# Kernel tuning notes

Hardware: AMD Instinct MI355X
Metric: run time of the kernel (lower is better)

## Reference

```python
import jax, jax.numpy as jnp
import numpy as np

MARGIN = 0.5
EPS = 1e-5
NOISE_RATE = 0.5


def setup_inputs() -> dict:
    key = jax.random.key(0)
    k1, k2, k3, k4, k5 = jax.random.split(key, 5)
    n, m, d, c = 1024, 65536, 512, 10000
    return {
        "inputs_col": jax.random.normal(k1, (n, d), dtype=jnp.float32),
        "inputs_row": jax.random.normal(k2, (m, d), dtype=jnp.float32),
        "center": jax.random.normal(k3, (c, d), dtype=jnp.float32),
        "targets_col": jax.random.randint(k4, (n,), 0, c, dtype=jnp.int64),
        "target_row": jax.random.randint(k5, (m,), 0, c, dtype=jnp.int64),
        "filled_mask": jnp.ones((c,), dtype=bool),
    }


def _prism_keep(features, targets, center, filled_mask, noise_rate):
    # no_grad in the original -> stop_gradient here
    f = jax.lax.stop_gradient(features)
    c = jax.lax.stop_gradient(center)
    # all_sim_exp[cls] / sum(all_sim_exp) is exactly softmax over class logits
    probs = jax.nn.softmax(f @ c.T, axis=-1)          # [n, num_classes]
    sel = jnp.take_along_axis(probs, targets[:, None], axis=1)[:, 0]  # [n]
    C = jnp.where(filled_mask[targets], sel, 1.0)      # not-in-memory -> 1
    n = C.shape[0]
    n_remove = int(noise_rate * n)                     # static
    to_remove = jnp.argsort(C)[:n_remove]
    # empty margin_window path: keep everything except to_remove
    keep = jnp.ones((n,), dtype=bool).at[to_remove].set(False)
    return keep


def reference(inputs_col, inputs_row, center, targets_col, target_row, filled_mask):
    n = inputs_col.shape[0]
    sim = inputs_col @ inputs_row.T                    # [n, m]
    pos_mask = targets_col[:, None] == target_row[None, :]
    neg_mask = (~pos_mask) & (sim > MARGIN)
    pos_mask = pos_mask & (sim < 1.0 - EPS)

    keep = _prism_keep(inputs_col, targets_col, center, filled_mask, NOISE_RATE)
    pos_mask = pos_mask & keep[:, None]
    neg_mask = neg_mask & keep[:, None]

    # sum over selected pairs without boolean-indexing (masked reductions)
    pos_loss = jnp.sum(jnp.where(pos_mask, 1.0 - sim, 0.0))
    neg_loss = jnp.sum(jnp.where(neg_mask, sim, 0.0))
    loss = (pos_loss + neg_loss) / n
    return loss, keep
```

## Files before the change

### kernel.cpp

```cpp
#include <hip/hip_runtime.h>


typedef int    v4i   __attribute__((ext_vector_type(4)));
typedef float  f32x4 __attribute__((ext_vector_type(4)));
typedef unsigned char u8;

#define N_COL  1024
#define M_ROW  65536
#define DDIM   512
#define NCLS   10000
#define NT     79
#define NREM   512

#define OFF_A8   0u
#define OFF_C8   524288u
#define OFF_PMS  39256064u
#define OFF_LT   39903232u
#define OFF_COMP 39907328u
#define OFF_TCC  39909376u
#define OFF_ACC  39911424u
#define OFF_CNT  39911432u

__device__ __forceinline__ void async16(const void* g, void* l) {
    __builtin_amdgcn_global_load_lds(
        (const __attribute__((address_space(1))) void*)g,
        (__attribute__((address_space(3))) void*)l, 16, 0, 0);
}

__device__ __forceinline__ unsigned pack4_fp8(float4 v) {
    int r = 0;
    r = __builtin_amdgcn_cvt_pk_fp8_f32(v.x, v.y, r, false);
    r = __builtin_amdgcn_cvt_pk_fp8_f32(v.z, v.w, r, true);
    return (unsigned)r;
}

__device__ __forceinline__ void gemm8_128(const u8* __restrict__ A,
                                          const u8* __restrict__ B,
                                          int m0, int n0,
                                          u8* As, u8* Bs, f32x4 (&acc)[4][4]) {
    const int tid = threadIdx.x, wid = tid >> 6, lane = tid & 63;
    const int wm = wid >> 1, wn = wid & 1;
    const int q = lane >> 4, lc = lane & 15;

    const u8* gA[4]; const u8* gB[4]; int voff[4];
#pragma unroll
    for (int s = 0; s < 4; ++s) {
        const int c  = wid * 256 + s * 64 + lane;
        const int r  = c >> 3;
        const int gs = (c & 7) ^ (r & 7);
        gA[s] = A + (size_t)(m0 + r) * DDIM + gs * 16;
        gB[s] = B + (size_t)(n0 + r) * DDIM + gs * 16;
        voff[s] = c * 16;
    }
#pragma unroll
    for (int i = 0; i < 4; ++i)
#pragma unroll
        for (int j = 0; j < 4; ++j) acc[i][j] = (f32x4){0.f, 0.f, 0.f, 0.f};

    for (int kt = 0; kt < 4; ++kt) {
        const int kb = kt * 128;
#pragma unroll
        for (int s = 0; s < 4; ++s) {
            async16(gA[s] + kb, As + voff[s]);
            async16(gB[s] + kb, Bs + voff[s]);
        }
        __syncthreads();
#pragma unroll
        for (int ks = 0; ks < 4; ++ks) {
            const int gg = ks * 2 + (q >> 1);
            const int bo = (q & 1) * 8;
            long long af[4], bv[4];
#pragma unroll
            for (int i = 0; i < 4; ++i) {
                const int rA = wm * 64 + i * 16 + lc;
                af[i] = *(const long long*)(As + (rA * 8 + (gg ^ (rA & 7))) * 16 + bo);
                const int rB = wn * 64 + i * 16 + lc;
                bv[i] = *(const long long*)(Bs + (rB * 8 + (gg ^ (rB & 7))) * 16 + bo);
            }
#pragma unroll
            for (int i = 0; i < 4; ++i)
#pragma unroll
                for (int j = 0; j < 4; ++j)
                    acc[i][j] = __builtin_amdgcn_mfma_f32_16x16x32_fp8_fp8(
                        af[i], bv[j], acc[i][j], 0, 0, 0);
        }
        __syncthreads();
    }
}

__global__ void k_prep(const float4* __restrict__ a4, const float4* __restrict__ c4,
                       const float* __restrict__ a32, const float* __restrict__ c32,
                       const int* __restrict__ tcol,
                       unsigned* __restrict__ A8w, uint2* __restrict__ C8w,
                       float* __restrict__ lt, double* __restrict__ accd,
                       unsigned* __restrict__ cnt) {
    const int b = blockIdx.x, tid = threadIdx.x;
    if (b == 0 && tid == 0) { *accd = 0.0; *cnt = 0u; }
    if (b < 256) {
        const int idx = b * 256 + tid;
        A8w[idx * 2]     = pack4_fp8(a4[idx * 2]);
        A8w[idx * 2 + 1] = pack4_fp8(a4[idx * 2 + 1]);
    } else if (b < 2784) {
        const int cidx = (b - 256) * 256 + tid;
        const int row  = cidx >> 6;
        uint2 o = make_uint2(0u, 0u);
        if (row < NCLS) {
            o.x = pack4_fp8(c4[cidx * 2]);
            o.y = pack4_fp8(c4[cidx * 2 + 1]);
        }
        C8w[cidx] = o;
    } else {
        const int w = (b - 2784) * 4 + (tid >> 6), lane = tid & 63;
        const int t = tcol[w];
        const float* ar = a32 + (size_t)w * DDIM;
        const float* cr = c32 + (size_t)t * DDIM;
        float s = 0.f;
#pragma unroll
        for (int k = 0; k < DDIM / 64; ++k) s += ar[lane + k * 64] * cr[lane + k * 64];
        for (int off = 32; off; off >>= 1) s += __shfl_down(s, off, 64);
        if (lane == 0) lt[w] = s;
    }
}

__global__ __launch_bounds__(256, 3) void k_mid(const u8* __restrict__ A8,
                                                const u8* __restrict__ C8,
                                                float2* __restrict__ pms) {
    const int b = blockIdx.x, tid = threadIdx.x;
    __shared__ __align__(16) u8 As[16384], Bs[16384];
    __shared__ float s_mm[128][2], s_ss[128][2];
    const int n_t = b >> 3, m0 = (b & 7) * 128, n0 = n_t * 128;
    f32x4 acc[4][4];
    gemm8_128(A8, C8, m0, n0, As, Bs, acc);

    const int wid = tid >> 6, lane = tid & 63;
    const int wm = wid >> 1, wn = wid & 1, q = lane >> 4, lc = lane & 15;
    const int cbase = n0 + wn * 64 + lc;
#pragma unroll
    for (int i = 0; i < 4; ++i) {
#pragma unroll
        for (int reg = 0; reg < 4; ++reg) {
            float mm = -INFINITY, ss = 0.f;
#pragma unroll
            for (int j = 0; j < 4; ++j)
                if (cbase + j * 16 < NCLS) mm = fmaxf(mm, acc[i][j][reg]);
#pragma unroll
            for (int j = 0; j < 4; ++j)
                if (cbase + j * 16 < NCLS) ss += __expf(acc[i][j][reg] - mm);
#pragma unroll
            for (int d2 = 1; d2 < 16; d2 <<= 1) {
                float mo = __shfl_xor(mm, d2, 16);
                float so = __shfl_xor(ss, d2, 16);
                float M = fmaxf(mm, mo), S = 0.f;
                if (ss > 0.f) S += ss * __expf(mm - M);
                if (so > 0.f) S += so * __expf(mo - M);
                mm = M; ss = S;
            }
            if (lc == 0) {
                const int row = i * 16 + q * 4 + reg;
                s_mm[wm * 64 + row][wn] = mm;
                s_ss[wm * 64 + row][wn] = ss;
            }
        }
    }
    __syncthreads();
    if (tid < 128) {
        float m1 = s_mm[tid][0], s1 = s_ss[tid][0];
        float m2 = s_mm[tid][1], s2 = s_ss[tid][1];
        float M = fmaxf(m1, m2), S = 0.f;
        if (s1 > 0.f) S += s1 * __expf(m1 - M);
        if (s2 > 0.f) S += s2 * __expf(m2 - M);
        pms[(size_t)n_t * N_COL + m0 + tid] = make_float2(M, S);
    }
}

__global__ __launch_bounds__(1024) void k_sel(const float2* __restrict__ pms,
                                              const float* __restrict__ lt,
                                              const int* __restrict__ tcol,
                                              int* __restrict__ comp,
                                              int* __restrict__ tcc,
                                              float* __restrict__ keep_out) {
    __shared__ float v[N_COL];
    const int i = threadIdx.x;
    float M = -INFINITY, S = 0.f;
    for (int t = 0; t < NT; ++t) {
        float2 p = pms[(size_t)t * N_COL + i];
        if (p.y > 0.f) {
            if (p.x > M) { S = S * __expf(M - p.x) + p.y; M = p.x; }
            else         { S += p.y * __expf(p.x - M); }
        }
    }
    const float x = lt[i] - (M + logf(S));
    v[i] = x;
    __syncthreads();
    int rank = 0;
    const float4* v4 = (const float4*)v;
#pragma unroll 8
    for (int j4 = 0; j4 < N_COL / 4; ++j4) {
        float4 w = v4[j4];
        const int j = j4 * 4;
        rank += (w.x < x) || (w.x == x && j     < i);
        rank += (w.y < x) || (w.y == x && j + 1 < i);
        rank += (w.z < x) || (w.z == x && j + 2 < i);
        rank += (w.w < x) || (w.w == x && j + 3 < i);
    }
    const bool keep = rank >= NREM;
    keep_out[i] = keep ? 1.0f : 0.0f;
    if (keep) { comp[rank - NREM] = i; tcc[rank - NREM] = tcol[i]; }
}

__global__ __launch_bounds__(512, 2) void k_loss(const u8* __restrict__ A8,
                                                 const float4* __restrict__ brow4,
                                                 const int* __restrict__ comp,
                                                 const int* __restrict__ tcc,
                                                 const int* __restrict__ trow,
                                                 double* __restrict__ accd,
                                                 unsigned* __restrict__ cnt,
                                                 float* __restrict__ out) {
    __shared__ __align__(16) u8 As[2][32768];
    __shared__ __align__(16) u8 Bs[2][8192];
    __shared__ int s_map[512], s_tc[512], s_tr[128];
    __shared__ float s_red[8];
    const int b = blockIdx.x, tid = threadIdx.x;
    const int n0 = b * 128;
    s_map[tid] = comp[tid];
    s_tc[tid]  = tcc[tid];
    if (tid < 128) s_tr[tid] = trow[n0 + tid];
    __syncthreads();

    const int wid = tid >> 6, lane = tid & 63;
    const int wm = wid >> 1, wn = wid & 1;
    const int q = lane >> 4, lc = lane & 15;

    const u8* gA[4]; int vA[4];
#pragma unroll
    for (int s = 0; s < 4; ++s) {
        const int cc = s * 512 + tid;
        const int r  = cc >> 2, gs = (cc & 3) ^ (r & 3);
        gA[s] = A8 + (size_t)s_map[r] * DDIM + gs * 16;
        vA[s] = cc * 16;
    }
    const int rB0 = tid >> 2, gB0 = tid & 3;
    const float4* gB = brow4 + (size_t)(n0 + rB0) * (DDIM / 4) + gB0 * 4;
    const int vB = (rB0 * 4 + (gB0 ^ (rB0 & 3))) * 16;

    f32x4 acc[8][4];
#pragma unroll
    for (int i = 0; i < 8; ++i)
#pragma unroll
        for (int j = 0; j < 4; ++j) acc[i][j] = (f32x4){0.f, 0.f, 0.f, 0.f};

    auto compute = [&](const u8* Asc, const u8* Bsc) {
#pragma unroll
        for (int ks = 0; ks < 2; ++ks) {
            const int gg = ks * 2 + (q >> 1);
            const int bo = (q & 1) * 8;
            long long af[8], bv[4];
#pragma unroll
            for (int i = 0; i < 8; ++i) {
                const int rA = wm * 128 + i * 16 + lc;
                af[i] = *(const long long*)(Asc + (rA * 4 + (gg ^ (rA & 3))) * 16 + bo);
            }
#pragma unroll
            for (int j = 0; j < 4; ++j) {
                const int rB = wn * 64 + j * 16 + lc;
                bv[j] = *(const long long*)(Bsc + (rB * 4 + (gg ^ (rB & 3))) * 16 + bo);
            }
#pragma unroll
            for (int i = 0; i < 8; ++i)
#pragma unroll
                for (int j = 0; j < 4; ++j)
                    acc[i][j] = __builtin_amdgcn_mfma_f32_16x16x32_fp8_fp8(
                        af[i], bv[j], acc[i][j], 0, 0, 0);
        }
    };

    {
#pragma unroll
        for (int s = 0; s < 4; ++s) async16(gA[s], As[0] + vA[s]);
        float4 f0 = gB[0], f1 = gB[1], f2 = gB[2], f3 = gB[3];
        uint4 pk;
        pk.x = pack4_fp8(f0); pk.y = pack4_fp8(f1);
        pk.z = pack4_fp8(f2); pk.w = pack4_fp8(f3);
        *(uint4*)(Bs[0] + vB) = pk;
        __syncthreads();
    }
    int cur = 0;
    for (int kt = 0; kt < 7; ++kt) {
        const int nxt = cur ^ 1;
        const int kb  = (kt + 1) * 64;
#pragma unroll
        for (int s = 0; s < 4; ++s) async16(gA[s] + kb, As[nxt] + vA[s]);
        const float4* gb = gB + (size_t)(kt + 1) * 16;
        float4 f0 = gb[0], f1 = gb[1], f2 = gb[2], f3 = gb[3];

        compute(As[cur], Bs[cur]);

        uint4 pk;
        pk.x = pack4_fp8(f0); pk.y = pack4_fp8(f1);
        pk.z = pack4_fp8(f2); pk.w = pack4_fp8(f3);
        *(uint4*)(Bs[nxt] + vB) = pk;
        __syncthreads();
        cur = nxt;
    }
    compute(As[cur], Bs[cur]);

    const float POSMAX = 1.0f - 1e-5f;
    float local = 0.f;
#pragma unroll
    for (int i = 0; i < 8; ++i) {
#pragma unroll
        for (int j = 0; j < 4; ++j) {
            const int tr = s_tr[wn * 64 + j * 16 + lc];
#pragma unroll
            for (int reg = 0; reg < 4; ++reg) {
                const int row = wm * 128 + i * 16 + q * 4 + reg;
                const float sim = acc[i][j][reg];
                if (s_tc[row] == tr) {
                    if (sim < POSMAX) local += 1.0f - sim;
                } else if (sim > 0.5f) {
                    local += sim;
                }
            }
        }
    }
    for (int off = 32; off; off >>= 1) local += __shfl_down(local, off, 64);
    if (lane == 0) s_red[wid] = local;
    __syncthreads();
    if (tid == 0) {
        float blk = 0.f;
#pragma unroll
        for (int w = 0; w < 8; ++w) blk += s_red[w];
        atomicAdd(accd, (double)blk);
        __threadfence();
        if (atomicAdd(cnt, 1u) == 511u) {
            double vfin = atomicAdd(accd, 0.0);
            out[0] = (float)(vfin / (double)N_COL);
        }
    }
}

extern "C" void kernel_launch(void* const* d_in, const int* in_sizes, int n_in,
                              void* d_out, int out_size, void* d_ws, size_t ws_size,
                              hipStream_t stream) {
    (void)in_sizes; (void)n_in; (void)out_size; (void)ws_size;
    const float* inputs_col  = (const float*)d_in[0];
    const float* inputs_row  = (const float*)d_in[1];
    const float* center      = (const float*)d_in[2];
    const int*   targets_col = (const int*)d_in[3];
    const int*   target_row  = (const int*)d_in[4];
    float* out = (float*)d_out;
    char*  ws  = (char*)d_ws;

    u8*       A8   = (u8*)(ws + OFF_A8);
    u8*       C8   = (u8*)(ws + OFF_C8);
    float2*   pms  = (float2*)(ws + OFF_PMS);
    float*    lt   = (float*) (ws + OFF_LT);
    int*      comp = (int*)   (ws + OFF_COMP);
    int*      tcc  = (int*)   (ws + OFF_TCC);
    double*   accd = (double*)(ws + OFF_ACC);
    unsigned* cnt  = (unsigned*)(ws + OFF_CNT);

    k_prep<<<3040, 256, 0, stream>>>((const float4*)inputs_col, (const float4*)center,
                                     inputs_col, center, targets_col,
                                     (unsigned*)A8, (uint2*)C8, lt, accd, cnt);
    k_mid<<<632, 256, 0, stream>>>(A8, C8, pms);
    k_sel<<<1, 1024, 0, stream>>>(pms, lt, targets_col, comp, tcc, out + 1);
    k_loss<<<512, 512, 0, stream>>>(A8, (const float4*)inputs_row,
                                    comp, tcc, target_row, accd, cnt, out);
}
```

Measured before the change: 332.4 us.

## Triple-buffer A tiles with prefetch distance two and change LDS swizzle

The fp8 GEMM main loop now keeps three shared-memory buffers for the A tiles and two register buffers for the B rows, so tiles are issued two k-steps ahead. Explicit vmcnt and lgkmcnt waits with raw s_barrier replace __syncthreads, and the loop is fully unrolled. The XOR swizzle of the 16-byte groups now uses (row>>1)&3 instead of row&3, to reduce LDS bank conflicts on the 8-byte fragment reads. The aim is to hide global-load latency behind MFMA work. The catch is that the extra 32KB A buffer raises LDS per block to about 114KB, which may allow only one block per CU instead of the two requested by launch_bounds.

```diff
diff --git a/kernel.cpp b/kernel.cpp
--- a/kernel.cpp
+++ b/kernel.cpp
@@ -216,7 +216,7 @@
                                                  double* __restrict__ accd,
                                                  unsigned* __restrict__ cnt,
                                                  float* __restrict__ out) {
-    __shared__ __align__(16) u8 As[2][32768];
+    __shared__ __align__(16) u8 As[3][32768];
     __shared__ __align__(16) u8 Bs[2][8192];
     __shared__ int s_map[512], s_tc[512], s_tr[128];
     __shared__ float s_red[8];
@@ -235,13 +235,14 @@
 #pragma unroll
     for (int s = 0; s < 4; ++s) {
         const int cc = s * 512 + tid;
-        const int r  = cc >> 2, gs = (cc & 3) ^ (r & 3);
-        gA[s] = A8 + (size_t)s_map[r] * DDIM + gs * 16;
+        const int r  = cc >> 2, gpos = cc & 3;
+        const int g  = gpos ^ ((r >> 1) & 3);
+        gA[s] = A8 + (size_t)s_map[r] * DDIM + g * 16;
         vA[s] = cc * 16;
     }
     const int rB0 = tid >> 2, gB0 = tid & 3;
     const float4* gB = brow4 + (size_t)(n0 + rB0) * (DDIM / 4) + gB0 * 4;
-    const int vB = (rB0 * 4 + (gB0 ^ (rB0 & 3))) * 16;
+    const int vB = (rB0 * 4 + (gB0 ^ ((rB0 >> 1) & 3))) * 16;
 
     f32x4 acc[8][4];
 #pragma unroll
@@ -258,12 +259,12 @@
 #pragma unroll
             for (int i = 0; i < 8; ++i) {
                 const int rA = wm * 128 + i * 16 + lc;
-                af[i] = *(const long long*)(Asc + (rA * 4 + (gg ^ (rA & 3))) * 16 + bo);
+                af[i] = *(const long long*)(Asc + (rA * 4 + (gg ^ ((rA >> 1) & 3))) * 16 + bo);
             }
 #pragma unroll
             for (int j = 0; j < 4; ++j) {
                 const int rB = wn * 64 + j * 16 + lc;
-                bv[j] = *(const long long*)(Bsc + (rB * 4 + (gg ^ (rB & 3))) * 16 + bo);
+                bv[j] = *(const long long*)(Bsc + (rB * 4 + (gg ^ ((rB >> 1) & 3))) * 16 + bo);
             }
 #pragma unroll
             for (int i = 0; i < 8; ++i)
@@ -274,35 +275,53 @@
         }
     };
 
+    float4 fb[2][4];
+
+#pragma unroll
+    for (int s = 0; s < 4; ++s) async16(gA[s], As[0] + vA[s]);
+#pragma unroll
+    for (int g = 0; g < 4; ++g) fb[0][g] = gB[g];
+    __builtin_amdgcn_sched_barrier(0);
+#pragma unroll
+    for (int s = 0; s < 4; ++s) async16(gA[s] + 64, As[1] + vA[s]);
+#pragma unroll
+    for (int g = 0; g < 4; ++g) fb[1][g] = gB[16 + g];
+    asm volatile("s_waitcnt vmcnt(8)" ::: "memory");
+    __builtin_amdgcn_sched_barrier(0);
     {
-#pragma unroll
-        for (int s = 0; s < 4; ++s) async16(gA[s], As[0] + vA[s]);
-        float4 f0 = gB[0], f1 = gB[1], f2 = gB[2], f3 = gB[3];
         uint4 pk;
-        pk.x = pack4_fp8(f0); pk.y = pack4_fp8(f1);
-        pk.z = pack4_fp8(f2); pk.w = pack4_fp8(f3);
+        pk.x = pack4_fp8(fb[0][0]); pk.y = pack4_fp8(fb[0][1]);
+        pk.z = pack4_fp8(fb[0][2]); pk.w = pack4_fp8(fb[0][3]);
         *(uint4*)(Bs[0] + vB) = pk;
-        __syncthreads();
-    }
-    int cur = 0;
-    for (int kt = 0; kt < 7; ++kt) {
-        const int nxt = cur ^ 1;
-        const int kb  = (kt + 1) * 64;
-#pragma unroll
-        for (int s = 0; s < 4; ++s) async16(gA[s] + kb, As[nxt] + vA[s]);
-        const float4* gb = gB + (size_t)(kt + 1) * 16;
-        float4 f0 = gb[0], f1 = gb[1], f2 = gb[2], f3 = gb[3];
-
-        compute(As[cur], Bs[cur]);
-
-        uint4 pk;
-        pk.x = pack4_fp8(f0); pk.y = pack4_fp8(f1);
-        pk.z = pack4_fp8(f2); pk.w = pack4_fp8(f3);
-        *(uint4*)(Bs[nxt] + vB) = pk;
-        __syncthreads();
-        cur = nxt;
-    }
-    compute(As[cur], Bs[cur]);
+    }
+    asm volatile("s_waitcnt lgkmcnt(0)" ::: "memory");
+    __builtin_amdgcn_s_barrier();
+
+#pragma unroll
+    for (int kt = 0; kt < 8; ++kt) {
+        if (kt < 6) {
+            const int kb = (kt + 2) * 64;
+#pragma unroll
+            for (int s = 0; s < 4; ++s) async16(gA[s] + kb, As[(kt + 2) % 3] + vA[s]);
+#pragma unroll
+            for (int g = 0; g < 4; ++g) fb[kt & 1][g] = gB[(kt + 2) * 16 + g];
+            asm volatile("s_waitcnt vmcnt(8)" ::: "memory");
+        } else if (kt == 6) {
+            asm volatile("s_waitcnt vmcnt(0)" ::: "memory");
+        }
+        __builtin_amdgcn_sched_barrier(0);
+        if (kt < 7) {
+            uint4 pk;
+            pk.x = pack4_fp8(fb[(kt + 1) & 1][0]); pk.y = pack4_fp8(fb[(kt + 1) & 1][1]);
+            pk.z = pack4_fp8(fb[(kt + 1) & 1][2]); pk.w = pack4_fp8(fb[(kt + 1) & 1][3]);
+            *(uint4*)(Bs[(kt + 1) & 1] + vB) = pk;
+        }
+        compute(As[kt % 3], Bs[kt & 1]);
+        if (kt < 7) {
+            asm volatile("s_waitcnt lgkmcnt(0)" ::: "memory");
+            __builtin_amdgcn_s_barrier();
+        }
+    }
 
     const float POSMAX = 1.0f - 1e-5f;
     float local = 0.f;
```

After: 337.3 us. No clear change (+1.5%).

## Raise loss-kernel occupancy, change LDS swizzle, add MFMA priority hints

Applied to the files above, without the earlier changes.

Raises launch bounds from 2 to 4 blocks per CU for the fused GEMM-loss kernel. Drops the shared-memory staging of the index and label arrays: labels are read straight from global memory into registers, and the reduction scratch reuses the A tile buffer. Changes the LDS XOR swizzle to key on row>>1 to cut bank conflicts for the 8-byte fragment reads. Also fully unrolls the k-loop and wraps the MFMA block in s_setprio. The tighter register budget (acc alone is 128 VGPRs) risks spills, and the 80KB of LDS per block may still cap how many blocks fit per CU.

```diff
diff --git a/kernel.cpp b/kernel.cpp
--- a/kernel.cpp
+++ b/kernel.cpp
@@ -208,7 +208,7 @@
     if (keep) { comp[rank - NREM] = i; tcc[rank - NREM] = tcol[i]; }
 }
 
-__global__ __launch_bounds__(512, 2) void k_loss(const u8* __restrict__ A8,
+__global__ __launch_bounds__(512, 4) void k_loss(const u8* __restrict__ A8,
                                                  const float4* __restrict__ brow4,
                                                  const int* __restrict__ comp,
                                                  const int* __restrict__ tcc,
@@ -218,14 +218,8 @@
                                                  float* __restrict__ out) {
     __shared__ __align__(16) u8 As[2][32768];
     __shared__ __align__(16) u8 Bs[2][8192];
-    __shared__ int s_map[512], s_tc[512], s_tr[128];
-    __shared__ float s_red[8];
     const int b = blockIdx.x, tid = threadIdx.x;
     const int n0 = b * 128;
-    s_map[tid] = comp[tid];
-    s_tc[tid]  = tcc[tid];
-    if (tid < 128) s_tr[tid] = trow[n0 + tid];
-    __syncthreads();
 
     const int wid = tid >> 6, lane = tid & 63;
     const int wm = wid >> 1, wn = wid & 1;
@@ -235,13 +229,14 @@
 #pragma unroll
     for (int s = 0; s < 4; ++s) {
         const int cc = s * 512 + tid;
-        const int r  = cc >> 2, gs = (cc & 3) ^ (r & 3);
-        gA[s] = A8 + (size_t)s_map[r] * DDIM + gs * 16;
+        const int r  = cc >> 2, gpos = cc & 3;
+        const int g  = gpos ^ ((r >> 1) & 3);
+        gA[s] = A8 + (size_t)comp[r] * DDIM + g * 16;
         vA[s] = cc * 16;
     }
     const int rB0 = tid >> 2, gB0 = tid & 3;
     const float4* gB = brow4 + (size_t)(n0 + rB0) * (DDIM / 4) + gB0 * 4;
-    const int vB = (rB0 * 4 + (gB0 ^ (rB0 & 3))) * 16;
+    const int vB = (rB0 * 4 + (gB0 ^ ((rB0 >> 1) & 3))) * 16;
 
     f32x4 acc[8][4];
 #pragma unroll
@@ -258,19 +253,21 @@
 #pragma unroll
             for (int i = 0; i < 8; ++i) {
                 const int rA = wm * 128 + i * 16 + lc;
-                af[i] = *(const long long*)(Asc + (rA * 4 + (gg ^ (rA & 3))) * 16 + bo);
+                af[i] = *(const long long*)(Asc + (rA * 4 + (gg ^ ((rA >> 1) & 3))) * 16 + bo);
             }
 #pragma unroll
             for (int j = 0; j < 4; ++j) {
                 const int rB = wn * 64 + j * 16 + lc;
-                bv[j] = *(const long long*)(Bsc + (rB * 4 + (gg ^ (rB & 3))) * 16 + bo);
-            }
+                bv[j] = *(const long long*)(Bsc + (rB * 4 + (gg ^ ((rB >> 1) & 3))) * 16 + bo);
+            }
+            __builtin_amdgcn_s_setprio(1);
 #pragma unroll
             for (int i = 0; i < 8; ++i)
 #pragma unroll
                 for (int j = 0; j < 4; ++j)
                     acc[i][j] = __builtin_amdgcn_mfma_f32_16x16x32_fp8_fp8(
                         af[i], bv[j], acc[i][j], 0, 0, 0);
+            __builtin_amdgcn_s_setprio(0);
         }
     };
 
@@ -284,38 +281,43 @@
         *(uint4*)(Bs[0] + vB) = pk;
         __syncthreads();
     }
-    int cur = 0;
+#pragma unroll
     for (int kt = 0; kt < 7; ++kt) {
-        const int nxt = cur ^ 1;
-        const int kb  = (kt + 1) * 64;
-#pragma unroll
-        for (int s = 0; s < 4; ++s) async16(gA[s] + kb, As[nxt] + vA[s]);
+        const int kb = (kt + 1) * 64;
+#pragma unroll
+        for (int s = 0; s < 4; ++s) async16(gA[s] + kb, As[(kt + 1) & 1] + vA[s]);
         const float4* gb = gB + (size_t)(kt + 1) * 16;
         float4 f0 = gb[0], f1 = gb[1], f2 = gb[2], f3 = gb[3];
 
-        compute(As[cur], Bs[cur]);
+        compute(As[kt & 1], Bs[kt & 1]);
 
         uint4 pk;
         pk.x = pack4_fp8(f0); pk.y = pack4_fp8(f1);
         pk.z = pack4_fp8(f2); pk.w = pack4_fp8(f3);
-        *(uint4*)(Bs[nxt] + vB) = pk;
+        *(uint4*)(Bs[(kt + 1) & 1] + vB) = pk;
         __syncthreads();
-        cur = nxt;
-    }
-    compute(As[cur], Bs[cur]);
+    }
+    compute(As[1], Bs[1]);
+    __syncthreads();
+
+    int trj[4];
+#pragma unroll
+    for (int j = 0; j < 4; ++j) trj[j] = trow[n0 + wn * 64 + j * 16 + lc];
 
     const float POSMAX = 1.0f - 1e-5f;
     float local = 0.f;
 #pragma unroll
     for (int i = 0; i < 8; ++i) {
+        int tcr[4];
+#pragma unroll
+        for (int reg = 0; reg < 4; ++reg)
+            tcr[reg] = tcc[wm * 128 + i * 16 + q * 4 + reg];
 #pragma unroll
         for (int j = 0; j < 4; ++j) {
-            const int tr = s_tr[wn * 64 + j * 16 + lc];
 #pragma unroll
             for (int reg = 0; reg < 4; ++reg) {
-                const int row = wm * 128 + i * 16 + q * 4 + reg;
                 const float sim = acc[i][j][reg];
-                if (s_tc[row] == tr) {
+                if (tcr[reg] == trj[j]) {
                     if (sim < POSMAX) local += 1.0f - sim;
                 } else if (sim > 0.5f) {
                     local += sim;
@@ -324,6 +326,7 @@
         }
     }
     for (int off = 32; off; off >>= 1) local += __shfl_down(local, off, 64);
+    float* s_red = (float*)As;
     if (lane == 0) s_red[wid] = local;
     __syncthreads();
     if (tid == 0) {
```

Result: slower. 619.5 us (+86.3%).

## Fuse keep-rank selection into loss kernel and change LDS swizzle pattern

Applied to the files above, without the earlier changes.

The single-block selection kernel is split up. A small 16-block kernel now computes per-row log-softmax values, and every loss block recomputes the O(n^2) rank selection redundantly in shared memory to build its compacted row map, with block 0 writing the keep mask. This removes the serialized one-block launch and its global round trip, at the cost of duplicated rank work in all 512 loss blocks and more shared memory per block. The LDS XOR swizzle is also changed from (r&3) to ((r>>1)&3) to alter bank-conflict behavior for the 8-byte fragment reads.

```diff
diff --git a/kernel.cpp b/kernel.cpp
--- a/kernel.cpp
+++ b/kernel.cpp
@@ -16,8 +16,7 @@
 #define OFF_C8   524288u
 #define OFF_PMS  39256064u
 #define OFF_LT   39903232u
-#define OFF_COMP 39907328u
-#define OFF_TCC  39909376u
+#define OFF_LOGC 39907328u
 #define OFF_ACC  39911424u
 #define OFF_CNT  39911432u
 
@@ -173,14 +172,10 @@
     }
 }
 
-__global__ __launch_bounds__(1024) void k_sel(const float2* __restrict__ pms,
-                                              const float* __restrict__ lt,
-                                              const int* __restrict__ tcol,
-                                              int* __restrict__ comp,
-                                              int* __restrict__ tcc,
-                                              float* __restrict__ keep_out) {
-    __shared__ float v[N_COL];
-    const int i = threadIdx.x;
+__global__ void k_lse(const float2* __restrict__ pms,
+                      const float* __restrict__ lt,
+                      float* __restrict__ logc) {
+    const int i = blockIdx.x * 64 + threadIdx.x;
     float M = -INFINITY, S = 0.f;
     for (int t = 0; t < NT; ++t) {
         float2 p = pms[(size_t)t * N_COL + i];
@@ -189,42 +184,56 @@
             else         { S += p.y * __expf(p.x - M); }
         }
     }
-    const float x = lt[i] - (M + logf(S));
-    v[i] = x;
-    __syncthreads();
-    int rank = 0;
-    const float4* v4 = (const float4*)v;
-#pragma unroll 8
-    for (int j4 = 0; j4 < N_COL / 4; ++j4) {
-        float4 w = v4[j4];
-        const int j = j4 * 4;
-        rank += (w.x < x) || (w.x == x && j     < i);
-        rank += (w.y < x) || (w.y == x && j + 1 < i);
-        rank += (w.z < x) || (w.z == x && j + 2 < i);
-        rank += (w.w < x) || (w.w == x && j + 3 < i);
-    }
-    const bool keep = rank >= NREM;
-    keep_out[i] = keep ? 1.0f : 0.0f;
-    if (keep) { comp[rank - NREM] = i; tcc[rank - NREM] = tcol[i]; }
+    logc[i] = lt[i] - (M + logf(S));
 }
 
 __global__ __launch_bounds__(512, 2) void k_loss(const u8* __restrict__ A8,
                                                  const float4* __restrict__ brow4,
-                                                 const int* __restrict__ comp,
-                                                 const int* __restrict__ tcc,
+                                                 const float* __restrict__ logc,
+                                                 const int* __restrict__ tcol,
                                                  const int* __restrict__ trow,
                                                  double* __restrict__ accd,
                                                  unsigned* __restrict__ cnt,
-                                                 float* __restrict__ out) {
+                                                 float* __restrict__ out,
+                                                 float* __restrict__ kout) {
     __shared__ __align__(16) u8 As[2][32768];
     __shared__ __align__(16) u8 Bs[2][8192];
+    __shared__ float v[N_COL];
     __shared__ int s_map[512], s_tc[512], s_tr[128];
     __shared__ float s_red[8];
     const int b = blockIdx.x, tid = threadIdx.x;
     const int n0 = b * 128;
-    s_map[tid] = comp[tid];
-    s_tc[tid]  = tcc[tid];
+
+    v[tid]       = logc[tid];
+    v[tid + 512] = logc[tid + 512];
     if (tid < 128) s_tr[tid] = trow[n0 + tid];
+    __syncthreads();
+    {
+        const float x0 = v[tid], x1 = v[tid + 512];
+        const int i1 = tid + 512;
+        int r0 = 0, r1 = 0;
+        const float4* v4 = (const float4*)v;
+#pragma unroll 8
+        for (int j4 = 0; j4 < N_COL / 4; ++j4) {
+            float4 w = v4[j4];
+            const int j = j4 * 4;
+            r0 += (w.x < x0) || (w.x == x0 && j     < tid);
+            r0 += (w.y < x0) || (w.y == x0 && j + 1 < tid);
+            r0 += (w.z < x0) || (w.z == x0 && j + 2 < tid);
+            r0 += (w.w < x0) || (w.w == x0 && j + 3 < tid);
+            r1 += (w.x < x1) || (w.x == x1 && j     < i1);
+            r1 += (w.y < x1) || (w.y == x1 && j + 1 < i1);
+            r1 += (w.z < x1) || (w.z == x1 && j + 2 < i1);
+            r1 += (w.w < x1) || (w.w == x1 && j + 3 < i1);
+        }
+        const bool k0 = r0 >= NREM, k1 = r1 >= NREM;
+        if (k0) { s_map[r0 - NREM] = tid; s_tc[r0 - NREM] = tcol[tid]; }
+        if (k1) { s_map[r1 - NREM] = i1;  s_tc[r1 - NREM] = tcol[i1];  }
+        if (b == 0) {
+            kout[tid] = k0 ? 1.0f : 0.0f;
+            kout[i1]  = k1 ? 1.0f : 0.0f;
+        }
+    }
     __syncthreads();
 
     const int wid = tid >> 6, lane = tid & 63;
@@ -235,13 +244,14 @@
 #pragma unroll
     for (int s = 0; s < 4; ++s) {
         const int cc = s * 512 + tid;
-        const int r  = cc >> 2, gs = (cc & 3) ^ (r & 3);
-        gA[s] = A8 + (size_t)s_map[r] * DDIM + gs * 16;
+        const int r  = cc >> 2, gpos = cc & 3;
+        const int g  = gpos ^ ((r >> 1) & 3);
+        gA[s] = A8 + (size_t)s_map[r] * DDIM + g * 16;
         vA[s] = cc * 16;
     }
     const int rB0 = tid >> 2, gB0 = tid & 3;
     const float4* gB = brow4 + (size_t)(n0 + rB0) * (DDIM / 4) + gB0 * 4;
-    const int vB = (rB0 * 4 + (gB0 ^ (rB0 & 3))) * 16;
+    const int vB = (rB0 * 4 + (gB0 ^ ((rB0 >> 1) & 3))) * 16;
 
     f32x4 acc[8][4];
 #pragma unroll
@@ -258,12 +268,12 @@
 #pragma unroll
             for (int i = 0; i < 8; ++i) {
                 const int rA = wm * 128 + i * 16 + lc;
-                af[i] = *(const long long*)(Asc + (rA * 4 + (gg ^ (rA & 3))) * 16 + bo);
+                af[i] = *(const long long*)(Asc + (rA * 4 + (gg ^ ((rA >> 1) & 3))) * 16 + bo);
             }
 #pragma unroll
             for (int j = 0; j < 4; ++j) {
                 const int rB = wn * 64 + j * 16 + lc;
-                bv[j] = *(const long long*)(Bsc + (rB * 4 + (gg ^ (rB & 3))) * 16 + bo);
+                bv[j] = *(const long long*)(Bsc + (rB * 4 + (gg ^ ((rB >> 1) & 3))) * 16 + bo);
             }
 #pragma unroll
             for (int i = 0; i < 8; ++i)
@@ -355,8 +365,7 @@
     u8*       C8   = (u8*)(ws + OFF_C8);
     float2*   pms  = (float2*)(ws + OFF_PMS);
     float*    lt   = (float*) (ws + OFF_LT);
-    int*      comp = (int*)   (ws + OFF_COMP);
-    int*      tcc  = (int*)   (ws + OFF_TCC);
+    float*    logc = (float*) (ws + OFF_LOGC);
     double*   accd = (double*)(ws + OFF_ACC);
     unsigned* cnt  = (unsigned*)(ws + OFF_CNT);
 
@@ -364,7 +373,8 @@
                                      inputs_col, center, targets_col,
                                      (unsigned*)A8, (uint2*)C8, lt, accd, cnt);
     k_mid<<<632, 256, 0, stream>>>(A8, C8, pms);
-    k_sel<<<1, 1024, 0, stream>>>(pms, lt, targets_col, comp, tcc, out + 1);
+    k_lse<<<16, 64, 0, stream>>>(pms, lt, logc);
     k_loss<<<512, 512, 0, stream>>>(A8, (const float4*)inputs_row,
-                                    comp, tcc, target_row, accd, cnt, out);
-}
+                                    logc, targets_col, target_row,
+                                    accd, cnt, out, out + 1);
+}
```

Result: slower. 367.8 us (+10.6%).
